# Optimization experiments

Hardware: AMD Instinct MI355X
Metric: run time of the kernel (lower is better)

Reference implementation:

```python
import jax, jax.numpy as jnp
import numpy as np

BS, C, H, W = 8, 64, 128, 128
KS = 3
SCALE = 2


def _pose_map(src_h, src_w, scale):
    # Vectorized version of positionKPN.pose_map (bilinear source coords).
    dst_h, dst_w = int(np.floor(src_h * scale)), int(np.floor(src_w * scale))
    scale_x, scale_y = float(src_w) / dst_w, float(src_h) / dst_h
    src_x = (np.arange(dst_w) + 0.5) * scale_x - 0.5
    src_y = (np.arange(dst_h) + 0.5) * scale_y - 0.5
    x0, y0 = np.floor(src_x), np.floor(src_y)
    inter_x = np.broadcast_to((x0 + 1).astype(np.int32)[None, :], (dst_h, dst_w))
    inter_y = np.broadcast_to((y0 + 1).astype(np.int32)[:, None], (dst_h, dst_w))
    fx = np.broadcast_to((src_x - x0).astype(np.float32)[None, :], (dst_h, dst_w))
    fy = np.broadcast_to((src_y - y0).astype(np.float32)[:, None], (dst_h, dst_w))
    pose = np.stack([fx, fy], axis=0).astype(np.float32)  # [2, dst_h, dst_w]
    return pose, np.ascontiguousarray(inter_y), np.ascontiguousarray(inter_x)


def setup_inputs() -> dict:
    key = jax.random.key(0)
    ks = jax.random.split(key, 8)
    pose, inter_y, inter_x = _pose_map(H, W, SCALE)
    s = 0.05
    return {
        "x": jax.random.normal(ks[0], (BS, C, H, W), dtype=jnp.float32),
        "scale": SCALE,
        "poseMap": jnp.asarray(pose),
        "interMapY": jnp.asarray(inter_y),
        "interMapX": jnp.asarray(inter_x),
        "W1": jax.random.normal(ks[1], (128, 2), dtype=jnp.float32) * s,
        "b1": jnp.zeros((128,), dtype=jnp.float32),
        "W2": jax.random.normal(ks[2], (256, 128), dtype=jnp.float32) * s,
        "b2": jnp.zeros((256,), dtype=jnp.float32),
        "W3": jax.random.normal(ks[3], (C * KS * KS, 256), dtype=jnp.float32) * s,
        "b3": jnp.zeros((C * KS * KS,), dtype=jnp.float32),
    }


def reference(x, scale, poseMap, interMapY, interMapX, W1, b1, W2, b2, W3, b3):
    bs, cs, h, w = x.shape
    ho, wo = interMapY.shape
    k2 = KS * KS
    # 1x1-conv MLP on position map -> per-pixel dynamic kernels.
    h1 = jax.nn.relu(jnp.einsum('oc,chw->ohw', W1, poseMap) + b1[:, None, None])
    h2 = jax.nn.relu(jnp.einsum('oc,chw->ohw', W2, h1) + b2[:, None, None])
    wgt = jnp.einsum('oc,chw->ohw', W3, h2) + b3[:, None, None]  # [cs*k2, ho, wo]
    wgt = wgt.reshape(cs, k2, ho, wo)
    # 3x3 patches gathered at source-grid centers interMap in [0, h] x [0, w]
    # (patch center y needs rows y-1..y+1 of x -> pad 1 before, 2 after).
    pad = KS // 2
    xp = jnp.pad(x, ((0, 0), (0, 0), (pad, pad + 1), (pad, pad + 1)))
    ky, kx = jnp.meshgrid(jnp.arange(KS), jnp.arange(KS), indexing='ij')
    Y = interMapY[None, :, :] + ky.reshape(k2, 1, 1)  # [k2, ho, wo]
    X = interMapX[None, :, :] + kx.reshape(k2, 1, 1)
    taps = xp[:, :, Y, X]  # [bs, cs, k2, ho, wo]
    out = jnp.einsum('bckyx,ckyx->bcyx', taps, wgt)  # per-pixel dynamic depthwise conv
    return out
```

## Files before the change

kernel.cpp:

```cpp
#include <hip/hip_runtime.h>

#define H_IN   128
#define W_IN   128
#define H_OUT  256
#define W_OUT  256
#define C_CH   64
#define B_SZ   8

typedef float vfloat4 __attribute__((ext_vector_type(4)));

__device__ __forceinline__ float rfl(float v) {
    return __uint_as_float(__builtin_amdgcn_readfirstlane(__float_as_uint(v)));
}

__global__ __launch_bounds__(576) void kpn_mlp(
    const float* __restrict__ pose,
    const float* __restrict__ W1,
    const float* __restrict__ b1,
    const float* __restrict__ W2,
    const float* __restrict__ b2,
    const float* __restrict__ W3,
    const float* __restrict__ b3,
    float* __restrict__ wgt4)
{
    __shared__ float h1[128];
    __shared__ float h2[256];

    const int p  = blockIdx.x;
    const int py = p >> 1, px = p & 1;
    const int t  = threadIdx.x;

    const float fx = pose[0 * H_OUT * W_OUT + py * W_OUT + px];
    const float fy = pose[1 * H_OUT * W_OUT + py * W_OUT + px];

    if (t < 128) {
        float a = W1[t * 2 + 0] * fx + W1[t * 2 + 1] * fy + b1[t];
        h1[t] = a > 0.f ? a : 0.f;
    }
    __syncthreads();

    if (t < 256) {
        float acc = b2[t];
        const float4* w = (const float4*)(W2 + t * 128);
        #pragma unroll 8
        for (int k = 0; k < 32; ++k) {
            float4 wv = w[k];
            acc += wv.x * h1[4 * k + 0] + wv.y * h1[4 * k + 1]
                 + wv.z * h1[4 * k + 2] + wv.w * h1[4 * k + 3];
        }
        h2[t] = acc > 0.f ? acc : 0.f;
    }
    __syncthreads();

    {
        float acc = b3[t];
        const float4* w = (const float4*)(W3 + t * 256);
        #pragma unroll 16
        for (int k = 0; k < 64; ++k) {
            float4 wv = w[k];
            acc += wv.x * h2[4 * k + 0] + wv.y * h2[4 * k + 1]
                 + wv.z * h2[4 * k + 2] + wv.w * h2[4 * k + 3];
        }
        const int c = t / 9, k = t - c * 9;
        wgt4[c * 48 + p * 12 + k] = acc;
    }
}

__global__ __launch_bounds__(256) void kpn_apply(
    const float* __restrict__ x,
    const float* __restrict__ wgt4,
    float* __restrict__ out)
{
    const int l  = threadIdx.x;
    const int wv = threadIdx.y;
    const int bc = blockIdx.y;
    const int c  = bc & 63;
    const int i0 = blockIdx.x * 16 + wv * 4;

    const float* xp = x + (size_t)bc * (H_IN * W_IN) + 2 * l;

    float2 v[7];
    #pragma unroll
    for (int r = 0; r < 7; ++r) {
        int rr = i0 - 1 + r;
        int rc = rr < 0 ? 0 : (rr > H_IN - 1 ? H_IN - 1 : rr);
        v[r] = *(const float2*)(xp + rc * W_IN);
    }

    float wt[4][9];
    const float* wp = wgt4 + c * 48;
    #pragma unroll
    for (int p = 0; p < 4; ++p) {
        float4 a = *(const float4*)(wp + p * 12);
        float4 b = *(const float4*)(wp + p * 12 + 4);
        float  g = wp[p * 12 + 8];
        wt[p][0] = rfl(a.x); wt[p][1] = rfl(a.y); wt[p][2] = rfl(a.z); wt[p][3] = rfl(a.w);
        wt[p][4] = rfl(b.x); wt[p][5] = rfl(b.y); wt[p][6] = rfl(b.z); wt[p][7] = rfl(b.w);
        wt[p][8] = rfl(g);
    }

    float M[7], A[7], B[7], D[7], E[7];
    #pragma unroll
    for (int r = 0; r < 7; ++r) {
        const int rr = i0 - 1 + r;
        const bool ok = ((unsigned)rr < (unsigned)H_IN);
        float ax = ok ? v[r].x : 0.f;
        float bx = ok ? v[r].y : 0.f;
        float m = __shfl_up(bx, 1, 64);   if (l == 0)  m = 0.f;
        float d = __shfl_down(ax, 1, 64); if (l == 63) d = 0.f;
        float e = __shfl_down(bx, 1, 64); if (l == 63) e = 0.f;
        M[r] = m; A[r] = ax; B[r] = bx; D[r] = d; E[r] = e;
    }

    float* op = out + ((size_t)bc * H_OUT + 2 * (size_t)i0) * W_OUT + 4 * l;

    #pragma unroll
    for (int q = 0; q < 4; ++q) {
        float ox0 = 0.f, ox1 = 0.f, ox2 = 0.f, ox3 = 0.f;
        float oy0 = 0.f, oy1 = 0.f, oy2 = 0.f, oy3 = 0.f;
        #pragma unroll
        for (int ky = 0; ky < 3; ++ky) {
            const int su = q + ky;
            const int sl = q + ky + 1;
            const float w0a = wt[0][3*ky+0], w0b = wt[0][3*ky+1], w0c = wt[0][3*ky+2];
            const float w1a = wt[1][3*ky+0], w1b = wt[1][3*ky+1], w1c = wt[1][3*ky+2];
            const float w2a = wt[2][3*ky+0], w2b = wt[2][3*ky+1], w2c = wt[2][3*ky+2];
            const float w3a = wt[3][3*ky+0], w3b = wt[3][3*ky+1], w3c = wt[3][3*ky+2];
            ox0 += w0a * M[su] + w0b * A[su] + w0c * B[su];
            ox1 += w1a * A[su] + w1b * B[su] + w1c * D[su];
            ox2 += w0a * A[su] + w0b * B[su] + w0c * D[su];
            ox3 += w1a * B[su] + w1b * D[su] + w1c * E[su];
            oy0 += w2a * M[sl] + w2b * A[sl] + w2c * B[sl];
            oy1 += w3a * A[sl] + w3b * B[sl] + w3c * D[sl];
            oy2 += w2a * A[sl] + w2b * B[sl] + w2c * D[sl];
            oy3 += w3a * B[sl] + w3b * D[sl] + w3c * E[sl];
        }
        vfloat4 r0 = { ox0, ox1, ox2, ox3 };
        vfloat4 r1 = { oy0, oy1, oy2, oy3 };
        __builtin_nontemporal_store(r0, (vfloat4*)op);
        __builtin_nontemporal_store(r1, (vfloat4*)(op + W_OUT));
        op += 2 * W_OUT;
    }
}

extern "C" void kernel_launch(void* const* d_in, const int* in_sizes, int n_in,
                              void* d_out, int out_size, void* d_ws, size_t ws_size,
                              hipStream_t stream) {
    const float* x      = (const float*)d_in[0];
    const float* pose   = (const float*)d_in[2];
    const float* W1     = (const float*)d_in[5];
    const float* b1     = (const float*)d_in[6];
    const float* W2     = (const float*)d_in[7];
    const float* b2     = (const float*)d_in[8];
    const float* W3     = (const float*)d_in[9];
    const float* b3     = (const float*)d_in[10];
    float*       out    = (float*)d_out;
    float*       wgt4   = (float*)d_ws;

    kpn_mlp<<<dim3(4), dim3(576), 0, stream>>>(pose, W1, b1, W2, b2, W3, b3, wgt4);
    kpn_apply<<<dim3(8, 512), dim3(64, 4), 0, stream>>>(x, wgt4, out);
}
```

Measured before the change: 53.44 us.

## Give each wave 16 input rows with rolling software-pipelined row loads

```diff
diff --git a/kernel.cpp b/kernel.cpp
--- a/kernel.cpp
+++ b/kernel.cpp
@@ -66,26 +66,16 @@
     }
 }
 
-__global__ __launch_bounds__(256) void kpn_apply(
+__global__ __launch_bounds__(256, 4) void kpn_apply(
     const float* __restrict__ x,
     const float* __restrict__ wgt4,
     float* __restrict__ out)
 {
-    const int l  = threadIdx.x;
-    const int wv = threadIdx.y;
-    const int bc = blockIdx.y;
-    const int c  = bc & 63;
-    const int i0 = blockIdx.x * 16 + wv * 4;
-
-    const float* xp = x + (size_t)bc * (H_IN * W_IN) + 2 * l;
-
-    float2 v[7];
-    #pragma unroll
-    for (int r = 0; r < 7; ++r) {
-        int rr = i0 - 1 + r;
-        int rc = rr < 0 ? 0 : (rr > H_IN - 1 ? H_IN - 1 : rr);
-        v[r] = *(const float2*)(xp + rc * W_IN);
-    }
+    const int l    = threadIdx.x;
+    const int wgid = blockIdx.x * 4 + threadIdx.y;
+    const int bc   = wgid >> 3;
+    const int i0   = (wgid & 7) * 16;
+    const int c    = bc & 63;
 
     float wt[4][9];
     const float* wp = wgt4 + c * 48;
@@ -99,41 +89,59 @@
         wt[p][8] = rfl(g);
     }
 
-    float M[7], A[7], B[7], D[7], E[7];
-    #pragma unroll
-    for (int r = 0; r < 7; ++r) {
-        const int rr = i0 - 1 + r;
+    const float* xp = x + (size_t)bc * (H_IN * W_IN) + 2 * l;
+    const int    R0 = i0 - 1;
+
+    float2 v[8];
+    float M[4], Ax[4], Bx[4], Dx[4], Ex[4];
+
+    auto issue = [&](int r) {
+        int rr = R0 + r;
+        int rc = rr < 0 ? 0 : (rr > H_IN - 1 ? H_IN - 1 : rr);
+        v[r & 7] = *(const float2*)(xp + rc * W_IN);
+    };
+    auto expand = [&](int r) {
+        const int rr = R0 + r;
         const bool ok = ((unsigned)rr < (unsigned)H_IN);
-        float ax = ok ? v[r].x : 0.f;
-        float bx = ok ? v[r].y : 0.f;
+        float ax = ok ? v[r & 7].x : 0.f;
+        float bx = ok ? v[r & 7].y : 0.f;
         float m = __shfl_up(bx, 1, 64);   if (l == 0)  m = 0.f;
         float d = __shfl_down(ax, 1, 64); if (l == 63) d = 0.f;
         float e = __shfl_down(bx, 1, 64); if (l == 63) e = 0.f;
-        M[r] = m; A[r] = ax; B[r] = bx; D[r] = d; E[r] = e;
-    }
+        const int s = r & 3;
+        M[s] = m; Ax[s] = ax; Bx[s] = bx; Dx[s] = d; Ex[s] = e;
+    };
+
+    #pragma unroll
+    for (int r = 0; r < 8; ++r) issue(r);
+    #pragma unroll
+    for (int r = 0; r < 3; ++r) expand(r);
 
     float* op = out + ((size_t)bc * H_OUT + 2 * (size_t)i0) * W_OUT + 4 * l;
 
     #pragma unroll
-    for (int q = 0; q < 4; ++q) {
+    for (int q = 0; q < 16; ++q) {
+        if (q + 8 < 19) issue(q + 8);
+        expand(q + 3);
+
         float ox0 = 0.f, ox1 = 0.f, ox2 = 0.f, ox3 = 0.f;
         float oy0 = 0.f, oy1 = 0.f, oy2 = 0.f, oy3 = 0.f;
         #pragma unroll
         for (int ky = 0; ky < 3; ++ky) {
-            const int su = q + ky;
-            const int sl = q + ky + 1;
+            const int su = (q + ky) & 3;
+            const int sl = (q + ky + 1) & 3;
             const float w0a = wt[0][3*ky+0], w0b = wt[0][3*ky+1], w0c = wt[0][3*ky+2];
             const float w1a = wt[1][3*ky+0], w1b = wt[1][3*ky+1], w1c = wt[1][3*ky+2];
             const float w2a = wt[2][3*ky+0], w2b = wt[2][3*ky+1], w2c = wt[2][3*ky+2];
             const float w3a = wt[3][3*ky+0], w3b = wt[3][3*ky+1], w3c = wt[3][3*ky+2];
-            ox0 += w0a * M[su] + w0b * A[su] + w0c * B[su];
-            ox1 += w1a * A[su] + w1b * B[su] + w1c * D[su];
-            ox2 += w0a * A[su] + w0b * B[su] + w0c * D[su];
-            ox3 += w1a * B[su] + w1b * D[su] + w1c * E[su];
-            oy0 += w2a * M[sl] + w2b * A[sl] + w2c * B[sl];
-            oy1 += w3a * A[sl] + w3b * B[sl] + w3c * D[sl];
-            oy2 += w2a * A[sl] + w2b * B[sl] + w2c * D[sl];
-            oy3 += w3a * B[sl] + w3b * D[sl] + w3c * E[sl];
+            ox0 += w0a * M[su]  + w0b * Ax[su] + w0c * Bx[su];
+            ox1 += w1a * Ax[su] + w1b * Bx[su] + w1c * Dx[su];
+            ox2 += w0a * Ax[su] + w0b * Bx[su] + w0c * Dx[su];
+            ox3 += w1a * Bx[su] + w1b * Dx[su] + w1c * Ex[su];
+            oy0 += w2a * M[sl]  + w2b * Ax[sl] + w2c * Bx[sl];
+            oy1 += w3a * Ax[sl] + w3b * Bx[sl] + w3c * Dx[sl];
+            oy2 += w2a * Ax[sl] + w2b * Bx[sl] + w2c * Dx[sl];
+            oy3 += w3a * Bx[sl] + w3b * Dx[sl] + w3c * Ex[sl];
         }
         vfloat4 r0 = { ox0, ox1, ox2, ox3 };
         vfloat4 r1 = { oy0, oy1, oy2, oy3 };
@@ -158,5 +166,5 @@
     float*       wgt4   = (float*)d_ws;
 
     kpn_mlp<<<dim3(4), dim3(576), 0, stream>>>(pose, W1, b1, W2, b2, W3, b3, wgt4);
-    kpn_apply<<<dim3(8, 512), dim3(64, 4), 0, stream>>>(x, wgt4, out);
+    kpn_apply<<<dim3(1024), dim3(64, 4), 0, stream>>>(x, wgt4, out);
 }
```

Measured after the change: 53.19 us. No clear change (-0.5%).
